# Kernel tuning notes

Measured on AMD Instinct MI355X. Metric: run time of the kernel, lower is better.

Reference implementation:

```python
import jax, jax.numpy as jnp
import numpy as np

D_MODEL = 1024
N_HEAD = 16
N_KV = 8
HEAD_DIM = D_MODEL // N_HEAD  # 64
ROPE_BASE = 10000.0


def _rope_tables(T, head_dim):
    inv_freq = 1.0 / (ROPE_BASE ** (jnp.arange(0, head_dim, 2, dtype=jnp.float32) / head_dim))
    pos = jnp.arange(T, dtype=jnp.float32)
    freqs = pos[:, None] * inv_freq[None, :]  # [T, head_dim//2]
    return jnp.sin(freqs), jnp.cos(freqs)


def _apply_rope(x, sin, cos):
    # x: [B, H, T, D]; sin/cos: [T, D//2] broadcast over B,H
    x1 = x[..., ::2]
    x2 = x[..., 1::2]
    y1 = x1 * cos - x2 * sin
    y2 = x1 * sin + x2 * cos
    return jnp.stack([y1, y2], axis=-1).reshape(x.shape)


def setup_inputs() -> dict:
    key = jax.random.key(0)
    ks = jax.random.split(key, 5)
    B, T = 2, 2048
    x = jax.random.normal(ks[0], (B, T, D_MODEL), dtype=jnp.float32)
    std = 0.02
    Wq = std * jax.random.normal(ks[1], (D_MODEL, D_MODEL), dtype=jnp.float32)
    Wk = std * jax.random.normal(ks[2], (N_KV * HEAD_DIM, D_MODEL), dtype=jnp.float32)
    Wv = std * jax.random.normal(ks[3], (N_KV * HEAD_DIM, D_MODEL), dtype=jnp.float32)
    Wo = std * jax.random.normal(ks[4], (D_MODEL, D_MODEL), dtype=jnp.float32)
    return {"x": x, "Wq": Wq, "Wk": Wk, "Wv": Wv, "Wo": Wo}


def reference(x, Wq, Wk, Wv, Wo):
    B, T, _ = x.shape
    G = N_HEAD // N_KV  # query heads per kv head (repeat_interleave grouping)

    # projections (bias-free Linear: x @ W.T)
    q = (x @ Wq.T).reshape(B, T, N_HEAD, HEAD_DIM).transpose(0, 2, 1, 3)  # [B,H,T,D]
    k = (x @ Wk.T).reshape(B, T, N_KV, HEAD_DIM).transpose(0, 2, 1, 3)   # [B,Hkv,T,D]
    v = (x @ Wv.T).reshape(B, T, N_KV, HEAD_DIM).transpose(0, 2, 1, 3)

    sin, cos = _rope_tables(T, HEAD_DIM)
    q = _apply_rope(q, sin, cos)
    k = _apply_rope(k, sin, cos)

    # GQA without materializing repeated K/V: group q heads by kv head.
    # repeat_interleave(dim=1) maps q head h -> kv head h // G.
    qg = q.reshape(B, N_KV, G, T, HEAD_DIM)
    scale = 1.0 / np.sqrt(HEAD_DIM)
    scores = jnp.einsum('bkgtd,bksd->bkgts', qg, k) * scale  # [B,Hkv,G,T,T]
    causal = jnp.tril(jnp.ones((T, T), dtype=bool))
    scores = jnp.where(causal, scores, jnp.float32(-1e30))
    attn = jax.nn.softmax(scores, axis=-1)
    y = jnp.einsum('bkgts,bksd->bkgtd', attn, v)              # [B,Hkv,G,T,D]
    y = y.reshape(B, N_HEAD, T, HEAD_DIM).transpose(0, 2, 1, 3).reshape(B, T, D_MODEL)
    return y @ Wo.T
```

## Files before the change

### kernel.cpp

```cpp
#include <hip/hip_runtime.h>
#include <cstdint>
#include <cstddef>

typedef __attribute__((ext_vector_type(8))) __bf16 bf16x8;
typedef __attribute__((ext_vector_type(4))) __bf16 bf16x4;
typedef __attribute__((ext_vector_type(4))) float f32x4;

#define DEVI __device__ __forceinline__

DEVI void gload_lds16(const void* g, void* l) {
    __builtin_amdgcn_global_load_lds((const __attribute__((address_space(1))) void*)g,
                                     (__attribute__((address_space(3))) void*)l, 16, 0, 0);
}

__global__ __launch_bounds__(256) void cvt_all(
    const float* __restrict__ x, const float* __restrict__ wq,
    const float* __restrict__ wk, const float* __restrict__ wv,
    const float* __restrict__ wo,
    bf16x4* __restrict__ xb, bf16x4* __restrict__ wqb, bf16x4* __restrict__ wkb,
    bf16x4* __restrict__ wvb, bf16x4* __restrict__ wob,
    float* __restrict__ sint, float* __restrict__ cost)
{
    int i = blockIdx.x * 256 + threadIdx.x;
    const int stride = gridDim.x * 256;
    for (int k = i; k < 65536; k += stride) {
        int t = k >> 5, p = k & 31;
        float inv = powf(10000.0f, -(float)p / 32.0f);
        float f = (float)t * inv;
        float s, c;
        sincosf(f, &s, &c);
        sint[k] = s;
        cost[k] = c;
    }
    for (; i < 1835008; i += stride) {
        const float4* s; bf16x4* d; int j;
        if (i < 1048576)      { s = (const float4*)x;  d = xb;  j = i; }
        else if (i < 1310720) { s = (const float4*)wq; d = wqb; j = i - 1048576; }
        else if (i < 1441792) { s = (const float4*)wk; d = wkb; j = i - 1310720; }
        else if (i < 1572864) { s = (const float4*)wv; d = wvb; j = i - 1441792; }
        else                  { s = (const float4*)wo; d = wob; j = i - 1572864; }
        float4 v = s[j];
        bf16x4 o = { (__bf16)v.x, (__bf16)v.y, (__bf16)v.z, (__bf16)v.w };
        d[j] = o;
    }
}

__global__ __launch_bounds__(256) void qkv_gemm(
    const __bf16* __restrict__ xb, const __bf16* __restrict__ wqb,
    const __bf16* __restrict__ wkb, const __bf16* __restrict__ wvb,
    const float* __restrict__ sint, const float* __restrict__ cost,
    __bf16* __restrict__ Qo, __bf16* __restrict__ Ko, __bf16* __restrict__ VTo)
{
    __shared__ __bf16 As[2][4096];
    __shared__ __bf16 Bs[2][4096];
    const int tid = threadIdx.x;
    const int lane = tid & 63;
    const int wid = tid >> 6;
    const int wm = (wid >> 1) * 32, wn = (wid & 1) * 32;
    const int m0 = blockIdx.y * 64;
    const int n0 = blockIdx.x * 64;

    const __bf16* bsrc;
    if (n0 < 1024)      bsrc = wqb + (size_t)n0 * 1024;
    else if (n0 < 1536) bsrc = wkb + (size_t)(n0 - 1024) * 1024;
    else                bsrc = wvb + (size_t)(n0 - 1536) * 1024;
    const __bf16* asrc = xb + (size_t)m0 * 1024;

    f32x4 acc[2][2] = {};
    const int sr = tid >> 3, sc = tid & 7;
    const int gsc = (sc ^ (sr & 7)) * 8;

#define STAGE(BUF, K0) do {                                                             \
    gload_lds16(asrc + (size_t)sr * 1024 + (K0) + gsc,        (char*)As[BUF] + sr * 128 + sc * 16); \
    gload_lds16(asrc + (size_t)(sr + 32) * 1024 + (K0) + gsc, (char*)As[BUF] + (sr + 32) * 128 + sc * 16); \
    gload_lds16(bsrc + (size_t)sr * 1024 + (K0) + gsc,        (char*)Bs[BUF] + sr * 128 + sc * 16); \
    gload_lds16(bsrc + (size_t)(sr + 32) * 1024 + (K0) + gsc, (char*)Bs[BUF] + (sr + 32) * 128 + sc * 16); \
} while (0)

    STAGE(0, 0);
    __syncthreads();

#pragma unroll 1
    for (int step = 0; step < 16; ++step) {
        const int cur = step & 1;
        if (step < 15) STAGE(cur ^ 1, (step + 1) * 64);
#pragma unroll
        for (int ks = 0; ks < 2; ++ks) {
            bf16x8 af[2], bfv[2];
#pragma unroll
            for (int i = 0; i < 2; ++i) {
                int ra = wm + i * 16 + (lane & 15);
                af[i] = *(const bf16x8*)((const char*)As[cur] + ra * 128 + (((ks * 4 + (lane >> 4)) ^ (ra & 7)) * 16));
                int rb = wn + i * 16 + (lane & 15);
                bfv[i] = *(const bf16x8*)((const char*)Bs[cur] + rb * 128 + (((ks * 4 + (lane >> 4)) ^ (rb & 7)) * 16));
            }
#pragma unroll
            for (int mi = 0; mi < 2; ++mi)
#pragma unroll
                for (int ni = 0; ni < 2; ++ni)
                    acc[mi][ni] = __builtin_amdgcn_mfma_f32_16x16x32_bf16(af[mi], bfv[ni], acc[mi][ni], 0, 0, 0);
        }
        __syncthreads();
    }
#undef STAGE

    const int rg = lane >> 4, cf = lane & 15;
#pragma unroll
    for (int mi = 0; mi < 2; ++mi) {
#pragma unroll
        for (int ni = 0; ni < 2; ++ni) {
            if (n0 >= 1536) {
                int n = n0 + wn + ni * 16 + cf;
                int nn = n - 1536;
                int kvh = nn >> 6, d = nn & 63;
                int m = m0 + wm + mi * 16 + rg * 4;
                int b = m >> 11;
                int t = m & 2047;
                bf16x4 o;
#pragma unroll
                for (int r = 0; r < 4; ++r) o[r] = (__bf16)acc[mi][ni][r];
                *(bf16x4*)(VTo + ((size_t)(b * 8 + kvh) * 64 + d) * 2048 + t) = o;
            } else {
#pragma unroll
                for (int r = 0; r < 4; ++r) {
                    float v = acc[mi][ni][r];
                    float pv = __shfl_xor(v, 1, 64);
                    int m = m0 + wm + mi * 16 + rg * 4 + r;
                    int n = n0 + wn + ni * 16 + cf;
                    int b = m >> 11;
                    int t = m & 2047;
                    if (n < 1024) {
                        int h = n >> 6, d = n & 63;
                        float s = sint[t * 32 + (d >> 1)], c = cost[t * 32 + (d >> 1)];
                        float o = (d & 1) ? (pv * s + v * c) : (v * c - pv * s);
                        Qo[((size_t)(b * 16 + h) * 2048 + t) * 64 + d] = (__bf16)(o * 0.125f);
                    } else {
                        int nn = n - 1024;
                        int h = nn >> 6, d = nn & 63;
                        float s = sint[t * 32 + (d >> 1)], c = cost[t * 32 + (d >> 1)];
                        float o = (d & 1) ? (pv * s + v * c) : (v * c - pv * s);
                        Ko[((size_t)(b * 8 + h) * 2048 + t) * 64 + d] = (__bf16)o;
                    }
                }
            }
        }
    }
}

__global__ __launch_bounds__(256, 2) void attn_fwd(
    const __bf16* __restrict__ Qg, const __bf16* __restrict__ Kg,
    const __bf16* __restrict__ VTg, __bf16* __restrict__ Yg)
{
    __shared__ char Ks[2][8192];
    __shared__ char Vs[2][8192];
    __shared__ char Pl[8192];
    const int tid = threadIdx.x;
    const int lane = tid & 63;
    const int w = tid >> 6;
    const int lin = blockIdx.x;
    const int xcd = lin & 7, g = (lin >> 3) & 3, p = lin >> 5;
    const int bh = xcd + 8 * g;
    const int b = bh >> 4, h = bh & 15, kvh = h >> 1;
    const size_t qbase = (size_t)(b * 16 + h) * 2048 * 64;
    const size_t kbase = (size_t)(b * 8 + kvh) * 2048 * 64;
    const int rg = lane >> 4, cf = lane & 15;
    char* pw = Pl + w * 2048;

    const int sr = tid >> 3;
    const int sc = tid & 7;
    const int gsc = (sc ^ (sr & 7)) * 8;

    const int Ja = p, Jb = 31 - p;
    bf16x8 pk0, pk1, pv0, pv1;

    bf16x8 ones;
#pragma unroll
    for (int e = 0; e < 8; ++e) ones[e] = (__bf16)1.0f;

#define PRE(NT) do {                                                                    \
    const int _n0 = (NT) * 64;                                                          \
    pk0 = *(const bf16x8*)(Kg + kbase + (size_t)(_n0 + sr) * 64 + gsc);                 \
    pk1 = *(const bf16x8*)(Kg + kbase + (size_t)(_n0 + sr + 32) * 64 + gsc);            \
    pv0 = *(const bf16x8*)(VTg + kbase + (size_t)sr * 2048 + _n0 + gsc);                \
    pv1 = *(const bf16x8*)(VTg + kbase + (size_t)(sr + 32) * 2048 + _n0 + gsc);         \
} while (0)
#define WRITE_LDS(BUF) do {                                                             \
    *(bf16x8*)(Ks[BUF] + tid * 16) = pk0;                                               \
    *(bf16x8*)(Ks[BUF] + (tid + 256) * 16) = pk1;                                       \
    *(bf16x8*)(Vs[BUF] + tid * 16) = pv0;                                               \
    *(bf16x8*)(Vs[BUF] + (tid + 256) * 16) = pv1;                                       \
} while (0)

    PRE(0);
    WRITE_LDS(0);
    __syncthreads();

    bf16x8 qf[2];
    f32x4 oacc[4], lacc;
    int J = Ja, nt = 0, cur = 0;

#pragma unroll 1
    for (int s = 0; s <= 32; ++s) {
        const int r0 = J * 64 + w * 16;
        if (nt == 0) {
#pragma unroll
            for (int ks = 0; ks < 2; ++ks)
                qf[ks] = *(const bf16x8*)(Qg + qbase + (size_t)(r0 + cf) * 64 + ks * 32 + rg * 8);
#pragma unroll
            for (int r = 0; r < 4; ++r) oacc[r] = f32x4{};
            lacc = f32x4{};
        }

        if (s < 32) {
            const int nnt = (nt == J) ? 0 : nt + 1;
            PRE(nnt);
        }

        {
            bf16x8 kf[2][4];
#pragma unroll
            for (int ks = 0; ks < 2; ++ks)
#pragma unroll
                for (int ni = 0; ni < 4; ++ni)
                    kf[ks][ni] = *(const bf16x8*)(Ks[cur] + (ni * 16 + cf) * 128 + (((ks * 4 + rg) ^ (cf & 7)) * 16));

            f32x4 sacc[4] = {};
            __builtin_amdgcn_s_setprio(1);
#pragma unroll
            for (int ks = 0; ks < 2; ++ks)
#pragma unroll
                for (int ni = 0; ni < 4; ++ni)
                    sacc[ni] = __builtin_amdgcn_mfma_f32_16x16x32_bf16(qf[ks], kf[ks][ni], sacc[ni], 0, 0, 0);
            __builtin_amdgcn_s_setprio(0);

            bf16x8 vf[2][4];
#pragma unroll
            for (int ks = 0; ks < 2; ++ks)
#pragma unroll
                for (int df = 0; df < 4; ++df)
                    vf[ks][df] = *(const bf16x8*)(Vs[cur] + (df * 16 + cf) * 128 + (((ks * 4 + rg) ^ (cf & 7)) * 16));

            if (nt == J) {
#pragma unroll
                for (int ni = 0; ni < 4; ++ni)
#pragma unroll
                    for (int r = 0; r < 4; ++r)
                        if (ni * 16 + cf > w * 16 + rg * 4 + r)
                            sacc[ni][r] = -3.0e38f;
            }

#pragma unroll
            for (int ni = 0; ni < 4; ++ni)
#pragma unroll
                for (int r = 0; r < 4; ++r)
                    sacc[ni][r] = __expf(sacc[ni][r]);

#pragma unroll
            for (int ni = 0; ni < 4; ++ni)
#pragma unroll
                for (int r = 0; r < 4; ++r) {
                    int pr = rg * 4 + r;
                    int pc = ni * 16 + cf;
                    *(__bf16*)(pw + pr * 128 + (((pc >> 3) ^ (pr & 7)) * 8 + (pc & 7)) * 2) =
                        (__bf16)sacc[ni][r];
                }

            __builtin_amdgcn_s_setprio(1);
#pragma unroll
            for (int ks = 0; ks < 2; ++ks) {
                bf16x8 pf = *(const bf16x8*)(pw + cf * 128 + (((ks * 4 + rg) ^ (cf & 7)) * 16));
#pragma unroll
                for (int df = 0; df < 4; ++df)
                    oacc[df] = __builtin_amdgcn_mfma_f32_16x16x32_bf16(pf, vf[ks][df], oacc[df], 0, 0, 0);
                lacc = __builtin_amdgcn_mfma_f32_16x16x32_bf16(pf, ones, lacc, 0, 0, 0);
            }
            __builtin_amdgcn_s_setprio(0);
        }

        if (nt == J) {
#pragma unroll
            for (int r = 0; r < 4; ++r) {
                float inv = 1.0f / lacc[r];
                int t = r0 + rg * 4 + r;
#pragma unroll
                for (int df = 0; df < 4; ++df)
                    Yg[((size_t)b * 2048 + t) * 1024 + h * 64 + df * 16 + cf] =
                        (__bf16)(oacc[df][r] * inv);
            }
        }

        if (s < 32) WRITE_LDS(cur ^ 1);
        __syncthreads();
        cur ^= 1;
        if (nt == J) { J = Jb; nt = 0; } else ++nt;
    }
#undef PRE
#undef WRITE_LDS
}

__global__ __launch_bounds__(256) void out_gemm(
    const __bf16* __restrict__ Yb, const __bf16* __restrict__ Wob, float* __restrict__ outp)
{
    __shared__ __bf16 As[2][8192];
    __shared__ __bf16 Bs[2][4096];
    const int tid = threadIdx.x;
    const int lane = tid & 63;
    const int wid = tid >> 6;
    const int wm = wid * 32;
    const int m0 = blockIdx.y * 128;
    const int n0 = blockIdx.x * 64;
    const __bf16* asrc = Yb + (size_t)m0 * 1024;
    const __bf16* bsrc = Wob + (size_t)n0 * 1024;

    f32x4 acc[2][4] = {};
    const int srow = tid >> 3, schunk = tid & 7;
    const int gc = (schunk ^ (srow & 7)) * 8;

#define STAGE(BUF, K0) do {                                                             \
    _Pragma("unroll") for (int it = 0; it < 4; ++it) {                                  \
        int r = srow + it * 32;                                                         \
        gload_lds16(asrc + (size_t)r * 1024 + (K0) + gc, (char*)As[BUF] + r * 128 + schunk * 16); \
    }                                                                                   \
    _Pragma("unroll") for (int it = 0; it < 2; ++it) {                                  \
        int r = srow + it * 32;                                                         \
        gload_lds16(bsrc + (size_t)r * 1024 + (K0) + gc, (char*)Bs[BUF] + r * 128 + schunk * 16); \
    }                                                                                   \
} while (0)

    STAGE(0, 0);
    __syncthreads();

#pragma unroll 1
    for (int step = 0; step < 16; ++step) {
        const int cur = step & 1;
        if (step < 15) STAGE(cur ^ 1, (step + 1) * 64);
#pragma unroll
        for (int ks = 0; ks < 2; ++ks) {
            bf16x8 af[2], bfv[4];
#pragma unroll
            for (int i = 0; i < 2; ++i) {
                int ra = wm + i * 16 + (lane & 15);
                af[i] = *(const bf16x8*)((const char*)As[cur] + ra * 128 + (((ks * 4 + (lane >> 4)) ^ (ra & 7)) * 16));
            }
#pragma unroll
            for (int i = 0; i < 4; ++i) {
                int rb = i * 16 + (lane & 15);
                bfv[i] = *(const bf16x8*)((const char*)Bs[cur] + rb * 128 + (((ks * 4 + (lane >> 4)) ^ (rb & 7)) * 16));
            }
#pragma unroll
            for (int mi = 0; mi < 2; ++mi)
#pragma unroll
                for (int ni = 0; ni < 4; ++ni)
                    acc[mi][ni] = __builtin_amdgcn_mfma_f32_16x16x32_bf16(af[mi], bfv[ni], acc[mi][ni], 0, 0, 0);
        }
        __syncthreads();
    }
#undef STAGE

    const int rg = lane >> 4, cf = lane & 15;
#pragma unroll
    for (int mi = 0; mi < 2; ++mi)
#pragma unroll
        for (int ni = 0; ni < 4; ++ni)
#pragma unroll
            for (int r = 0; r < 4; ++r) {
                int m = m0 + wm + mi * 16 + rg * 4 + r;
                int n = n0 + ni * 16 + cf;
                outp[(size_t)m * 1024 + n] = acc[mi][ni][r];
            }
}

extern "C" void kernel_launch(void* const* d_in, const int* in_sizes, int n_in,
                              void* d_out, int out_size, void* d_ws, size_t ws_size,
                              hipStream_t stream)
{
    const float* x  = (const float*)d_in[0];
    const float* wq = (const float*)d_in[1];
    const float* wk = (const float*)d_in[2];
    const float* wv = (const float*)d_in[3];
    const float* wo = (const float*)d_in[4];

    char* ws = (char*)d_ws;
    __bf16* xb  = (__bf16*)(ws + 0);
    __bf16* wqb = (__bf16*)(ws + 8388608);
    __bf16* wkb = (__bf16*)(ws + 10485760);
    __bf16* wvb = (__bf16*)(ws + 11534336);
    __bf16* wob = (__bf16*)(ws + 12582912);
    __bf16* Qb  = (__bf16*)(ws + 14680064);
    __bf16* Kb  = (__bf16*)(ws + 23068672);
    __bf16* VTb = (__bf16*)(ws + 31457280);
    __bf16* Yb  = (__bf16*)(ws + 35651584);
    float* sint = (float*)(ws + 44040192);
    float* cost = (float*)(ws + 44302336);
    if (ws_size < 44564480) return;

    cvt_all<<<2048, 256, 0, stream>>>(x, wq, wk, wv, wo,
                                      (bf16x4*)xb, (bf16x4*)wqb, (bf16x4*)wkb,
                                      (bf16x4*)wvb, (bf16x4*)wob, sint, cost);
    qkv_gemm<<<dim3(32, 64), 256, 0, stream>>>(xb, wqb, wkb, wvb, sint, cost, Qb, Kb, VTb);
    attn_fwd<<<512, 256, 0, stream>>>(Qb, Kb, VTb, Yb);
    out_gemm<<<dim3(16, 32), 256, 0, stream>>>(Yb, wob, (float*)d_out);
}
```

Measured before the change: 99.02 us.

## Enlarge QKV GEMM tile to 128x64 and hoist V fragment loads in attention

The QKV projection GEMM now uses a 128x64 block tile. Each of the four waves computes a 32x64 sub-tile, which doubles per-wave MFMA work and halves the grid to 32x32 blocks, so B tiles are reused across more rows and LDS traffic per FLOP drops. In the attention kernel, V fragment loads from LDS are issued together with the K loads, before the QK MFMAs, so their latency overlaps the matrix math. The trade-offs are more LDS and registers per block in the GEMM, fewer blocks for the CUs, and higher VGPR pressure in attention.

```diff
diff --git a/kernel.cpp b/kernel.cpp
--- a/kernel.cpp
+++ b/kernel.cpp
@@ -51,13 +51,13 @@
     const float* __restrict__ sint, const float* __restrict__ cost,
     __bf16* __restrict__ Qo, __bf16* __restrict__ Ko, __bf16* __restrict__ VTo)
 {
-    __shared__ __bf16 As[2][4096];
+    __shared__ __bf16 As[2][8192];
     __shared__ __bf16 Bs[2][4096];
     const int tid = threadIdx.x;
     const int lane = tid & 63;
     const int wid = tid >> 6;
-    const int wm = (wid >> 1) * 32, wn = (wid & 1) * 32;
-    const int m0 = blockIdx.y * 64;
+    const int wm = wid * 32;
+    const int m0 = blockIdx.y * 128;
     const int n0 = blockIdx.x * 64;
 
     const __bf16* bsrc;
@@ -66,15 +66,19 @@
     else                bsrc = wvb + (size_t)(n0 - 1536) * 1024;
     const __bf16* asrc = xb + (size_t)m0 * 1024;
 
-    f32x4 acc[2][2] = {};
-    const int sr = tid >> 3, sc = tid & 7;
-    const int gsc = (sc ^ (sr & 7)) * 8;
+    f32x4 acc[2][4] = {};
+    const int srow = tid >> 3, schunk = tid & 7;
+    const int gc = (schunk ^ (srow & 7)) * 8;
 
 #define STAGE(BUF, K0) do {                                                             \
-    gload_lds16(asrc + (size_t)sr * 1024 + (K0) + gsc,        (char*)As[BUF] + sr * 128 + sc * 16); \
-    gload_lds16(asrc + (size_t)(sr + 32) * 1024 + (K0) + gsc, (char*)As[BUF] + (sr + 32) * 128 + sc * 16); \
-    gload_lds16(bsrc + (size_t)sr * 1024 + (K0) + gsc,        (char*)Bs[BUF] + sr * 128 + sc * 16); \
-    gload_lds16(bsrc + (size_t)(sr + 32) * 1024 + (K0) + gsc, (char*)Bs[BUF] + (sr + 32) * 128 + sc * 16); \
+    _Pragma("unroll") for (int it = 0; it < 4; ++it) {                                  \
+        int r = srow + it * 32;                                                         \
+        gload_lds16(asrc + (size_t)r * 1024 + (K0) + gc, (char*)As[BUF] + r * 128 + schunk * 16); \
+    }                                                                                   \
+    _Pragma("unroll") for (int it = 0; it < 2; ++it) {                                  \
+        int r = srow + it * 32;                                                         \
+        gload_lds16(bsrc + (size_t)r * 1024 + (K0) + gc, (char*)Bs[BUF] + r * 128 + schunk * 16); \
+    }                                                                                   \
 } while (0)
 
     STAGE(0, 0);
@@ -86,18 +90,21 @@
         if (step < 15) STAGE(cur ^ 1, (step + 1) * 64);
 #pragma unroll
         for (int ks = 0; ks < 2; ++ks) {
-            bf16x8 af[2], bfv[2];
+            bf16x8 af[2], bfv[4];
 #pragma unroll
             for (int i = 0; i < 2; ++i) {
                 int ra = wm + i * 16 + (lane & 15);
                 af[i] = *(const bf16x8*)((const char*)As[cur] + ra * 128 + (((ks * 4 + (lane >> 4)) ^ (ra & 7)) * 16));
-                int rb = wn + i * 16 + (lane & 15);
+            }
+#pragma unroll
+            for (int i = 0; i < 4; ++i) {
+                int rb = i * 16 + (lane & 15);
                 bfv[i] = *(const bf16x8*)((const char*)Bs[cur] + rb * 128 + (((ks * 4 + (lane >> 4)) ^ (rb & 7)) * 16));
             }
 #pragma unroll
             for (int mi = 0; mi < 2; ++mi)
 #pragma unroll
-                for (int ni = 0; ni < 2; ++ni)
+                for (int ni = 0; ni < 4; ++ni)
                     acc[mi][ni] = __builtin_amdgcn_mfma_f32_16x16x32_bf16(af[mi], bfv[ni], acc[mi][ni], 0, 0, 0);
         }
         __syncthreads();
@@ -108,9 +115,9 @@
 #pragma unroll
     for (int mi = 0; mi < 2; ++mi) {
 #pragma unroll
-        for (int ni = 0; ni < 2; ++ni) {
+        for (int ni = 0; ni < 4; ++ni) {
             if (n0 >= 1536) {
-                int n = n0 + wn + ni * 16 + cf;
+                int n = n0 + ni * 16 + cf;
                 int nn = n - 1536;
                 int kvh = nn >> 6, d = nn & 63;
                 int m = m0 + wm + mi * 16 + rg * 4;
@@ -126,7 +133,7 @@
                     float v = acc[mi][ni][r];
                     float pv = __shfl_xor(v, 1, 64);
                     int m = m0 + wm + mi * 16 + rg * 4 + r;
-                    int n = n0 + wn + ni * 16 + cf;
+                    int n = n0 + ni * 16 + cf;
                     int b = m >> 11;
                     int t = m & 2047;
                     if (n < 1024) {
@@ -217,12 +224,17 @@
         }
 
         {
-            bf16x8 kf[2][4];
+            bf16x8 kf[2][4], vf[2][4];
 #pragma unroll
             for (int ks = 0; ks < 2; ++ks)
 #pragma unroll
                 for (int ni = 0; ni < 4; ++ni)
                     kf[ks][ni] = *(const bf16x8*)(Ks[cur] + (ni * 16 + cf) * 128 + (((ks * 4 + rg) ^ (cf & 7)) * 16));
+#pragma unroll
+            for (int ks = 0; ks < 2; ++ks)
+#pragma unroll
+                for (int df = 0; df < 4; ++df)
+                    vf[ks][df] = *(const bf16x8*)(Vs[cur] + (df * 16 + cf) * 128 + (((ks * 4 + rg) ^ (cf & 7)) * 16));
 
             f32x4 sacc[4] = {};
             __builtin_amdgcn_s_setprio(1);
@@ -232,13 +244,6 @@
                 for (int ni = 0; ni < 4; ++ni)
                     sacc[ni] = __builtin_amdgcn_mfma_f32_16x16x32_bf16(qf[ks], kf[ks][ni], sacc[ni], 0, 0, 0);
             __builtin_amdgcn_s_setprio(0);
-
-            bf16x8 vf[2][4];
-#pragma unroll
-            for (int ks = 0; ks < 2; ++ks)
-#pragma unroll
-                for (int df = 0; df < 4; ++df)
-                    vf[ks][df] = *(const bf16x8*)(Vs[cur] + (df * 16 + cf) * 128 + (((ks * 4 + rg) ^ (cf & 7)) * 16));
 
             if (nt == J) {
 #pragma unroll
@@ -397,7 +402,7 @@
     cvt_all<<<2048, 256, 0, stream>>>(x, wq, wk, wv, wo,
                                       (bf16x4*)xb, (bf16x4*)wqb, (bf16x4*)wkb,
                                       (bf16x4*)wvb, (bf16x4*)wob, sint, cost);
-    qkv_gemm<<<dim3(32, 64), 256, 0, stream>>>(xb, wqb, wkb, wvb, sint, cost, Qb, Kb, VTb);
+    qkv_gemm<<<dim3(32, 32), 256, 0, stream>>>(xb, wqb, wkb, wvb, sint, cost, Qb, Kb, VTb);
     attn_fwd<<<512, 256, 0, stream>>>(Qb, Kb, VTb, Yb);
     out_gemm<<<dim3(16, 32), 256, 0, stream>>>(Yb, wob, (float*)d_out);
 }
```

Result: slower. 102.3 us (+3.3%).
